# Kernel optimization log

Measured on AMD Instinct MI355X. Metric: run time of the kernel, lower is better.

Reference implementation:

```python
import jax, jax.numpy as jnp
import numpy as np

EPS_R2 = 1e-12
EPS_POS = 1e-08
EPS_SUM = 1e-12


def _gaussian_psf(k, sigma):
    ax = np.arange(-k // 2 + 1.0, k // 2 + 1.0)
    xx, yy = np.meshgrid(ax, ax)
    g = np.exp(-(xx ** 2 + yy ** 2) / (2.0 * sigma ** 2))
    g = g / g.sum()
    return jnp.asarray(g.astype(np.float32))[None, None]  # (1,1,k,k)


def setup_inputs() -> dict:
    key = jax.random.key(0)
    k1, k2, k3 = jax.random.split(key, 3)
    B, C, H, W = 16, 1, 1024, 1024
    src = jax.random.normal(k1, (B, C, H, W), dtype=jnp.float32)
    raw_psf = _gaussian_psf(21, 3.0) + 0.001 * jax.random.normal(k2, (1, 1, 21, 21), dtype=jnp.float32)
    sub = 0.1 * jax.random.normal(k3, (2,), dtype=jnp.float32)
    return {
        "src": src,
        "raw_psf": raw_psf,
        "x0": jnp.float32(0.0),
        "y0": jnp.float32(0.0),
        "raw_b": jnp.float32(0.08),
        "raw_rc": jnp.float32(0.01),
        "raw_subpix": sub,
    }


def _bilinear_sample(src, gx, gy):
    # src: (B,C,H,W); gx, gy: (B,Hg,Wg) normalized coords in [-1,1],
    # align_corners=True, zeros padding (matches F.grid_sample).
    B, C, H, W = src.shape
    ix = (gx + 1.0) * 0.5 * (W - 1)
    iy = (gy + 1.0) * 0.5 * (H - 1)
    ix0 = jnp.floor(ix)
    iy0 = jnp.floor(iy)
    wx1 = ix - ix0
    wy1 = iy - iy0
    ix0i = ix0.astype(jnp.int32)
    iy0i = iy0.astype(jnp.int32)
    ix1i = ix0i + 1
    iy1i = iy0i + 1
    bidx = jnp.arange(B)[:, None, None]

    def corner(yi, xi, w):
        valid = (yi >= 0) & (yi < H) & (xi >= 0) & (xi < W)
        yc = jnp.clip(yi, 0, H - 1)
        xc = jnp.clip(xi, 0, W - 1)
        v = src[bidx, :, yc, xc]  # (B,Hg,Wg,C)
        return v * (w * valid)[..., None]

    out = (corner(iy0i, ix0i, (1.0 - wy1) * (1.0 - wx1))
           + corner(iy0i, ix1i, (1.0 - wy1) * wx1)
           + corner(iy1i, ix0i, wy1 * (1.0 - wx1))
           + corner(iy1i, ix1i, wy1 * wx1))
    return jnp.transpose(out, (0, 3, 1, 2))  # (B,C,Hg,Wg)


def reference(src, raw_psf, x0, y0, raw_b, raw_rc, raw_subpix):
    B, C, H, W = src.shape
    k = raw_psf.shape[-1]
    b = jax.nn.softplus(raw_b) + EPS_POS
    rc = jax.nn.softplus(raw_rc) + EPS_POS
    sub = 0.25 * jnp.tanh(raw_subpix)

    xs = jnp.linspace(-1.0, 1.0, W)
    ys = jnp.linspace(-1.0, 1.0, H)
    # torch.meshgrid(ys, xs, indexing='xy') semantics: shape (W, H),
    # yv[i,j] = ys[j], xv[i,j] = xs[i] (note: transposed vs usual HxW).
    yv, xv = jnp.meshgrid(ys, xs, indexing='xy')

    dx = xv - x0
    dy = yv - y0
    denom = jnp.sqrt(dx * dx + dy * dy + EPS_R2 + rc * rc)
    ax = b * dx / denom
    ay = b * dy / denom

    gx = jnp.broadcast_to(xv - ax + sub[0], (B, W, H))
    gy = jnp.broadcast_to(yv - ay + sub[1], (B, W, H))

    y_warp = _bilinear_sample(src, gx, gy)  # (B,C,W,H)

    psf = jnp.maximum(raw_psf, 0.0)
    psf = psf / jnp.maximum(psf.sum(axis=(2, 3), keepdims=True), EPS_SUM)
    pad = k // 2
    y_conv = jax.lax.conv_general_dilated(
        y_warp, psf, window_strides=(1, 1),
        padding=((pad, pad), (pad, pad)),
        dimension_numbers=("NCHW", "OIHW", "NCHW"))
    return y_conv
```

## Files before the change

### kernel.cpp

```cpp
#include <hip/hip_runtime.h>
#include <math.h>

#define WW 1024
#define HH 1024
#define TI 64
#define TJ 128
#define HALO_J 148
#define VALID_I 84
#define FILL_I 96
#define PITCH_T 104
#define AOFF 448
#define AOFF2 21952
#define YOFF 43520
#define NEED_WS (174080u + 33554432u)

typedef short short8 __attribute__((ext_vector_type(8)));
typedef float float16 __attribute__((ext_vector_type(16)));

__device__ __forceinline__ unsigned short f2bf(float f) {
    union { float f; unsigned int u; } c; c.f = f;
    unsigned int u = c.u;
    return (unsigned short)((u + 0x7FFFu + ((u >> 16) & 1u)) >> 16);
}

__device__ __forceinline__ float warp_sample(const float* __restrict__ sb, int I, int J,
                                             float bpar, float rc2, float sub0, float sub1,
                                             float x0, float y0) {
    const float SSTEP = 2.0f / 1023.0f;
    float yv = fmaf((float)J, SSTEP, -1.0f);
    float xv = fmaf((float)I, SSTEP, -1.0f);
    float dx = xv - x0;
    float dy = yv - y0;
    float s = bpar * __builtin_amdgcn_rsqf(dx * dx + dy * dy + rc2);
    float gx = xv - dx * s + sub0;
    float gy = yv - dy * s + sub1;
    float ix = (gx + 1.0f) * (0.5f * 1023.0f);
    float iy = (gy + 1.0f) * (0.5f * 1023.0f);
    float fx = floorf(ix), fy = floorf(iy);
    float wx1 = ix - fx, wy1 = iy - fy;
    float wx0 = 1.f - wx1, wy0 = 1.f - wy1;
    int xi0 = (int)fx, yi0 = (int)fy;
    int xi1 = xi0 + 1, yi1 = yi0 + 1;
    int xc0 = min(max(xi0, 0), WW - 1);
    int xc1 = min(max(xi1, 0), WW - 1);
    int yc0 = min(max(yi0, 0), HH - 1);
    int yc1 = min(max(yi1, 0), HH - 1);
    bool vx0 = (unsigned)xi0 < WW, vx1 = (unsigned)xi1 < WW;
    bool vy0 = (unsigned)yi0 < HH, vy1 = (unsigned)yi1 < HH;
    float w00 = (vx0 && vy0) ? wy0 * wx0 : 0.f;
    float w01 = (vx1 && vy0) ? wy0 * wx1 : 0.f;
    float w10 = (vx0 && vy1) ? wy1 * wx0 : 0.f;
    float w11 = (vx1 && vy1) ? wy1 * wx1 : 0.f;
    float v00 = sb[yc0 * WW + xc0];
    float v01 = sb[yc0 * WW + xc1];
    float v10 = sb[yc1 * WW + xc0];
    float v11 = sb[yc1 * WW + xc1];
    return v00 * w00 + v01 * w01 + v10 * w10 + v11 * w11;
}

__global__ void prep_kernel(const float* __restrict__ raw_psf,
                            const float* __restrict__ x0p, const float* __restrict__ y0p,
                            const float* __restrict__ raw_b, const float* __restrict__ raw_rc,
                            const float* __restrict__ raw_sub,
                            float* __restrict__ ws) {
    __shared__ float red[512];
    __shared__ float psn[441];
    int t = threadIdx.x;
    float v = 0.f;
    if (t < 441) v = fmaxf(raw_psf[t], 0.f);
    red[t] = v;
    __syncthreads();
    for (int s = 256; s > 0; s >>= 1) {
        if (t < s) red[t] += red[t + s];
        __syncthreads();
    }
    float sum = fmaxf(red[0], 1e-12f);
    if (t < 441) { float pn = v / sum; ws[t] = pn; psn[t] = pn; }
    if (t == 0) {
        float b  = log1pf(expf(raw_b[0]))  + 1e-8f;
        float rc = log1pf(expf(raw_rc[0])) + 1e-8f;
        ws[441] = b;
        ws[442] = 1e-12f + rc * rc;
        ws[443] = 0.25f * tanhf(raw_sub[0]);
        ws[444] = 0.25f * tanhf(raw_sub[1]);
        ws[445] = x0p[0];
        ws[446] = y0p[0];
    }
    __syncthreads();

    short* A  = (short*)(ws + AOFF);
    short* A2 = (short*)(ws + AOFF2);
    for (int g = t; g < 21 * 256; g += 512) {
        int vv = g >> 8;
        int r  = g & 255;
        int d  = r >> 6;
        int l  = r & 63;
        int m  = l & 31;
        int k0 = (l >> 5) << 3;
        short8 o8, o8b;
#pragma unroll
        for (int q = 0; q < 8; ++q) {
            int u = 16 * d + k0 + q - m;
            unsigned short pv = 0, pv2 = 0;
            if ((unsigned)u <= 20u) pv = f2bf(psn[u * 21 + vv]);
            int u2 = u - 6;
            if ((unsigned)u2 <= 20u) pv2 = f2bf(psn[u2 * 21 + vv]);
            o8[q]  = (short)pv;
            o8b[q] = (short)pv2;
        }
        *(short8*)&A[(size_t)g * 8]  = o8;
        *(short8*)&A2[(size_t)g * 8] = o8b;
    }
}

__global__ __launch_bounds__(256, 4) void warp_kernel(
        const float* __restrict__ src, const float* __restrict__ pp,
        unsigned short* __restrict__ yw) {
    const float bpar = pp[441], rc2 = pp[442];
    const float sub0 = pp[443], sub1 = pp[444];
    const float x0 = pp[445], y0 = pp[446];
    const float SSTEP = 2.0f / 1023.0f;

    const int tid = threadIdx.x;
    const int nb  = blockIdx.x;
    const int b0  = nb >> 7;
    const int J0  = (nb & 127) << 3;
    const float* sb = src + ((size_t)b0 << 20);
    unsigned short* yb = yw + ((size_t)b0 << 20) + ((size_t)J0 << 10);

#pragma unroll 1
    for (int jr = 0; jr < 8; ++jr) {
        int J = J0 + jr;
        float yv = fmaf((float)J, SSTEP, -1.0f);
        float dy = yv - y0;
        float dyt = fmaf(dy, dy, rc2);
        unsigned short* yrow = yb + (jr << 10);

        float ixa[4], iya[4];
        bool bad = false;
#pragma unroll
        for (int q = 0; q < 4; ++q) {
            int I = (q << 8) + tid;
            float xv = fmaf((float)I, SSTEP, -1.0f);
            float dx = xv - x0;
            float s  = bpar * __builtin_amdgcn_rsqf(fmaf(dx, dx, dyt));
            float gx = xv - dx * s + sub0;
            float gy = yv - dy * s + sub1;
            ixa[q] = (gx + 1.0f) * (0.5f * 1023.0f);
            iya[q] = (gy + 1.0f) * (0.5f * 1023.0f);
            bad |= !(ixa[q] >= 0.f && ixa[q] < 1023.f &&
                     iya[q] >= 0.f && iya[q] < 1023.f);
        }
        if (!__any(bad)) {
            float v00[4], v01[4], v10[4], v11[4], fxs[4], fys[4];
#pragma unroll
            for (int q = 0; q < 4; ++q) {
                float fx = floorf(ixa[q]), fy = floorf(iya[q]);
                fxs[q] = fx; fys[q] = fy;
                const float* p = sb + (((int)fy) << 10) + (int)fx;
                v00[q] = p[0];
                v01[q] = p[1];
                v10[q] = p[WW];
                v11[q] = p[WW + 1];
            }
#pragma unroll
            for (int q = 0; q < 4; ++q) {
                float wx1 = ixa[q] - fxs[q];
                float wy1 = iya[q] - fys[q];
                float wx0 = 1.f - wx1;
                float r0 = fmaf(wx1, v01[q], wx0 * v00[q]);
                float r1 = fmaf(wx1, v11[q], wx0 * v10[q]);
                float val = fmaf(wy1, r1, (1.f - wy1) * r0);
                yrow[(q << 8) + tid] = f2bf(val);
            }
        } else {
#pragma unroll
            for (int q = 0; q < 4; ++q) {
                int I = (q << 8) + tid;
                float val = warp_sample(sb, I, J, bpar, rc2, sub0, sub1, x0, y0);
                yrow[(q << 8) + tid] = f2bf(val);
            }
        }
    }
}

__global__ __launch_bounds__(256, 5) void conv_kernel(
        const unsigned short* __restrict__ yw, const float* __restrict__ pp,
        float* __restrict__ out) {
    __shared__ unsigned short ThT[HALO_J * PITCH_T];

    const int tid = threadIdx.x;
    const int j0 = blockIdx.x * TJ;
    const int i0 = blockIdx.y * TI;
    const int b0 = blockIdx.z;

    const int lane = tid & 63;
    const int wv = tid >> 6;
    const int nrow = lane & 31;
    const int khalf = lane >> 5;

    const short8* Ap = ((const short8*)(pp + AOFF2)) + lane;
    short8 AfA[4], AfB[4];
#pragma unroll
    for (int d = 0; d < 4; ++d) AfA[d] = Ap[d * 64];
#pragma unroll
    for (int d = 0; d < 4; ++d) AfB[d] = Ap[256 + d * 64];

    const unsigned short* wb = yw + ((size_t)b0 << 20);

    for (int p = tid; p < HALO_J * 12; p += 256) {
        int hc = (int)((unsigned)p / 12u);
        int c  = p - hc * 12;
        int J  = j0 - 10 + hc;
        int xs = i0 - 16 + c * 8;
        short8 d8 = {0, 0, 0, 0, 0, 0, 0, 0};
        if ((unsigned)J < HH && (unsigned)xs < WW)
            d8 = *(const short8*)&wb[J * WW + xs];
        *(short8*)&ThT[hc * PITCH_T + c * 8] = d8;
    }
    __syncthreads();

    float16 acc[2];
#pragma unroll
    for (int m = 0; m < 2; ++m)
#pragma unroll
        for (int q = 0; q < 16; ++q) acc[m][q] = 0.f;

    const unsigned short* bpbase = &ThT[(32 * wv + nrow) * PITCH_T + khalf * 8];

#pragma unroll 1
    for (int v = 0; v < 20; v += 2) {
        {
            short8 Cur[4];
#pragma unroll
            for (int d = 0; d < 4; ++d) Cur[d] = AfA[d];
            int vp = v + 2;
#pragma unroll
            for (int d = 0; d < 4; ++d) AfA[d] = Ap[vp * 256 + d * 64];

            const unsigned short* bp = bpbase + v * PITCH_T;
            short8 Bf[6];
#pragma unroll
            for (int c = 0; c < 6; ++c) Bf[c] = *(const short8*)&bp[16 * c];
#pragma unroll
            for (int mq = 0; mq < 2; ++mq)
#pragma unroll
                for (int d = 0; d < 4; ++d)
                    acc[mq] = __builtin_amdgcn_mfma_f32_32x32x16_bf16(
                        Cur[d], Bf[2 * mq + d], acc[mq], 0, 0, 0);
        }
        {
            short8 Cur[4];
#pragma unroll
            for (int d = 0; d < 4; ++d) Cur[d] = AfB[d];
            int vp = v + 3; vp = vp > 20 ? 20 : vp;
#pragma unroll
            for (int d = 0; d < 4; ++d) AfB[d] = Ap[vp * 256 + d * 64];

            const unsigned short* bp = bpbase + (v + 1) * PITCH_T;
            short8 Bf[6];
#pragma unroll
            for (int c = 0; c < 6; ++c) Bf[c] = *(const short8*)&bp[16 * c];
#pragma unroll
            for (int mq = 0; mq < 2; ++mq)
#pragma unroll
                for (int d = 0; d < 4; ++d)
                    acc[mq] = __builtin_amdgcn_mfma_f32_32x32x16_bf16(
                        Cur[d], Bf[2 * mq + d], acc[mq], 0, 0, 0);
        }
    }
    {
        const unsigned short* bp = bpbase + 20 * PITCH_T;
        short8 Bf[6];
#pragma unroll
        for (int c = 0; c < 6; ++c) Bf[c] = *(const short8*)&bp[16 * c];
#pragma unroll
        for (int mq = 0; mq < 2; ++mq)
#pragma unroll
            for (int d = 0; d < 4; ++d)
                acc[mq] = __builtin_amdgcn_mfma_f32_32x32x16_bf16(
                    AfA[d], Bf[2 * mq + d], acc[mq], 0, 0, 0);
    }

    float* ob = out + (size_t)b0 * (WW * (size_t)HH);
    const int gj = j0 + 32 * wv + nrow;
#pragma unroll
    for (int mq = 0; mq < 2; ++mq) {
#pragma unroll
        for (int reg = 0; reg < 16; ++reg) {
            int row = (reg & 3) + 8 * (reg >> 2) + 4 * khalf;
            int gi = i0 + 32 * mq + row;
            ob[(size_t)gi * HH + gj] = acc[mq][reg];
        }
    }
}

__global__ __launch_bounds__(256, 4) void fused_kernel(
        const float* __restrict__ src, const float* __restrict__ pp,
        float* __restrict__ out) {
    __shared__ unsigned short ThT[HALO_J * PITCH_T];

    const int tid = threadIdx.x;
    const int j0 = blockIdx.x * TJ;
    const int i0 = blockIdx.y * TI;
    const int b0 = blockIdx.z;

    const float bpar = pp[441], rc2 = pp[442];
    const float sub0 = pp[443], sub1 = pp[444];
    const float x0 = pp[445], y0 = pp[446];

    const float* sb = src + (size_t)b0 * (HH * (size_t)WW);

    const int NELEM = HALO_J * FILL_I;
#pragma unroll 1
    for (int base = 0; base < NELEM; base += 1024) {
        float vals[4];
        int offs[4];
#pragma unroll
        for (int e = 0; e < 4; ++e) {
            int n = base + (e << 8) + tid;
            float val = 0.f;
            int off = -1;
            if (n < NELEM) {
                int hc = (int)((unsigned)n / 96u);
                int hr = n - hc * 96;
                off = hc * PITCH_T + hr;
                int J = j0 - 10 + hc;
                int I = i0 - 10 + hr;
                if (hr < VALID_I && (unsigned)J < HH && (unsigned)I < WW)
                    val = warp_sample(sb, I, J, bpar, rc2, sub0, sub1, x0, y0);
            }
            vals[e] = val;
            offs[e] = off;
        }
#pragma unroll
        for (int e = 0; e < 4; ++e) {
            if (offs[e] >= 0) ThT[offs[e]] = f2bf(vals[e]);
        }
    }
    __syncthreads();

    const int lane = tid & 63;
    const int wv = tid >> 6;
    const int nrow = lane & 31;
    const int khalf = lane >> 5;

    float16 acc[2];
#pragma unroll
    for (int m = 0; m < 2; ++m)
#pragma unroll
        for (int q = 0; q < 16; ++q) acc[m][q] = 0.f;

    const short8* Aall = (const short8*)(pp + AOFF);

#pragma unroll 1
    for (int v = 0; v < 21; ++v) {
        short8 Af[4];
#pragma unroll
        for (int d = 0; d < 4; ++d)
            Af[d] = Aall[(v * 4 + d) * 64 + lane];

        const unsigned short* bp = &ThT[(32 * wv + nrow + v) * PITCH_T + khalf * 8];
        short8 Bf[6];
#pragma unroll
        for (int c = 0; c < 6; ++c)
            Bf[c] = *(const short8*)&bp[16 * c];

#pragma unroll
        for (int mq = 0; mq < 2; ++mq) {
#pragma unroll
            for (int d = 0; d < 4; ++d)
                acc[mq] = __builtin_amdgcn_mfma_f32_32x32x16_bf16(
                    Af[d], Bf[2 * mq + d], acc[mq], 0, 0, 0);
        }
    }

    float* ob = out + (size_t)b0 * (WW * (size_t)HH);
    const int gj = j0 + 32 * wv + nrow;
#pragma unroll
    for (int mq = 0; mq < 2; ++mq) {
#pragma unroll
        for (int reg = 0; reg < 16; ++reg) {
            int row = (reg & 3) + 8 * (reg >> 2) + 4 * khalf;
            int gi = i0 + 32 * mq + row;
            ob[(size_t)gi * HH + gj] = acc[mq][reg];
        }
    }
}

extern "C" void kernel_launch(void* const* d_in, const int* in_sizes, int n_in,
                              void* d_out, int out_size, void* d_ws, size_t ws_size,
                              hipStream_t stream) {
    const float* src     = (const float*)d_in[0];
    const float* raw_psf = (const float*)d_in[1];
    const float* x0      = (const float*)d_in[2];
    const float* y0      = (const float*)d_in[3];
    const float* raw_b   = (const float*)d_in[4];
    const float* raw_rc  = (const float*)d_in[5];
    const float* raw_sub = (const float*)d_in[6];
    float* ws = (float*)d_ws;

    prep_kernel<<<1, 512, 0, stream>>>(raw_psf, x0, y0, raw_b, raw_rc, raw_sub, ws);

    dim3 grid(HH / TJ, WW / TI, 16);
    if (ws_size >= (size_t)NEED_WS) {
        unsigned short* yw = (unsigned short*)(ws + YOFF);
        warp_kernel<<<2048, 256, 0, stream>>>(src, ws, yw);
        conv_kernel<<<grid, 256, 0, stream>>>(yw, ws, (float*)d_out);
    } else {
        fused_kernel<<<grid, 256, 0, stream>>>(src, ws, (float*)d_out);
    }
}
```

Baseline: 191.0 us.

## Batch two rows per warp iteration and software-pipeline LDS loads in conv

The warp kernel now handles two output rows per iteration, issuing eight gather groups at once with a scheduling barrier so more global loads are in flight before the interpolation math. The conv kernel double-buffers its B fragments read from shared memory, loading the next row's fragments and A weights while the current MFMAs run, so LDS latency is hidden behind matrix work. Conv launch bounds drop from 5 to 4 waves per SIMD to leave room for the extra live registers. This raises register pressure and may reduce occupancy in both kernels.

```diff
diff --git a/kernel.cpp b/kernel.cpp
--- a/kernel.cpp
+++ b/kernel.cpp
@@ -129,62 +129,72 @@
     unsigned short* yb = yw + ((size_t)b0 << 20) + ((size_t)J0 << 10);
 
 #pragma unroll 1
-    for (int jr = 0; jr < 8; ++jr) {
-        int J = J0 + jr;
-        float yv = fmaf((float)J, SSTEP, -1.0f);
-        float dy = yv - y0;
-        float dyt = fmaf(dy, dy, rc2);
-        unsigned short* yrow = yb + (jr << 10);
-
-        float ixa[4], iya[4];
+    for (int jp = 0; jp < 4; ++jp) {
+        const int Jr = J0 + 2 * jp;
+        float yv0 = fmaf((float)Jr, SSTEP, -1.0f);
+        float yv1 = fmaf((float)(Jr + 1), SSTEP, -1.0f);
+        float dy0 = yv0 - y0, dy1 = yv1 - y0;
+        float dyt0 = fmaf(dy0, dy0, rc2), dyt1 = fmaf(dy1, dy1, rc2);
+        unsigned short* yrow0 = yb + ((2 * jp) << 10);
+        unsigned short* yrow1 = yrow0 + 1024;
+
+        float ixa[8], iya[8];
         bool bad = false;
 #pragma unroll
-        for (int q = 0; q < 4; ++q) {
+        for (int e = 0; e < 8; ++e) {
+            int r = e >> 2, q = e & 3;
             int I = (q << 8) + tid;
+            float yv  = r ? yv1 : yv0;
+            float dy  = r ? dy1 : dy0;
+            float dyt = r ? dyt1 : dyt0;
             float xv = fmaf((float)I, SSTEP, -1.0f);
             float dx = xv - x0;
             float s  = bpar * __builtin_amdgcn_rsqf(fmaf(dx, dx, dyt));
             float gx = xv - dx * s + sub0;
             float gy = yv - dy * s + sub1;
-            ixa[q] = (gx + 1.0f) * (0.5f * 1023.0f);
-            iya[q] = (gy + 1.0f) * (0.5f * 1023.0f);
-            bad |= !(ixa[q] >= 0.f && ixa[q] < 1023.f &&
-                     iya[q] >= 0.f && iya[q] < 1023.f);
+            ixa[e] = (gx + 1.0f) * (0.5f * 1023.0f);
+            iya[e] = (gy + 1.0f) * (0.5f * 1023.0f);
+            bad |= !(ixa[e] >= 0.f && ixa[e] < 1023.f &&
+                     iya[e] >= 0.f && iya[e] < 1023.f);
         }
         if (!__any(bad)) {
-            float v00[4], v01[4], v10[4], v11[4], fxs[4], fys[4];
-#pragma unroll
-            for (int q = 0; q < 4; ++q) {
-                float fx = floorf(ixa[q]), fy = floorf(iya[q]);
-                fxs[q] = fx; fys[q] = fy;
+            float v00[8], v01[8], v10[8], v11[8], fxs[8], fys[8];
+#pragma unroll
+            for (int e = 0; e < 8; ++e) {
+                float fx = floorf(ixa[e]), fy = floorf(iya[e]);
+                fxs[e] = fx; fys[e] = fy;
                 const float* p = sb + (((int)fy) << 10) + (int)fx;
-                v00[q] = p[0];
-                v01[q] = p[1];
-                v10[q] = p[WW];
-                v11[q] = p[WW + 1];
+                v00[e] = p[0];
+                v01[e] = p[1];
+                v10[e] = p[WW];
+                v11[e] = p[WW + 1];
             }
-#pragma unroll
-            for (int q = 0; q < 4; ++q) {
-                float wx1 = ixa[q] - fxs[q];
-                float wy1 = iya[q] - fys[q];
+            __builtin_amdgcn_sched_barrier(0);
+#pragma unroll
+            for (int e = 0; e < 8; ++e) {
+                float wx1 = ixa[e] - fxs[e];
+                float wy1 = iya[e] - fys[e];
                 float wx0 = 1.f - wx1;
-                float r0 = fmaf(wx1, v01[q], wx0 * v00[q]);
-                float r1 = fmaf(wx1, v11[q], wx0 * v10[q]);
+                float r0 = fmaf(wx1, v01[e], wx0 * v00[e]);
+                float r1 = fmaf(wx1, v11[e], wx0 * v10[e]);
                 float val = fmaf(wy1, r1, (1.f - wy1) * r0);
-                yrow[(q << 8) + tid] = f2bf(val);
+                unsigned short* yr = (e >> 2) ? yrow1 : yrow0;
+                yr[((e & 3) << 8) + tid] = f2bf(val);
             }
         } else {
 #pragma unroll
-            for (int q = 0; q < 4; ++q) {
-                int I = (q << 8) + tid;
+            for (int e = 0; e < 8; ++e) {
+                int I = ((e & 3) << 8) + tid;
+                int J = Jr + (e >> 2);
                 float val = warp_sample(sb, I, J, bpar, rc2, sub0, sub1, x0, y0);
-                yrow[(q << 8) + tid] = f2bf(val);
+                unsigned short* yr = (e >> 2) ? yrow1 : yrow0;
+                yr[((e & 3) << 8) + tid] = f2bf(val);
             }
         }
     }
 }
 
-__global__ __launch_bounds__(256, 5) void conv_kernel(
+__global__ __launch_bounds__(256, 4) void conv_kernel(
         const unsigned short* __restrict__ yw, const float* __restrict__ pp,
         float* __restrict__ out) {
     __shared__ unsigned short ThT[HALO_J * PITCH_T];
@@ -228,59 +238,61 @@
 
     const unsigned short* bpbase = &ThT[(32 * wv + nrow) * PITCH_T + khalf * 8];
 
+    short8 BfA[6], BfB[6];
+#pragma unroll
+    for (int c = 0; c < 6; ++c) BfA[c] = *(const short8*)&bpbase[16 * c];
+#pragma unroll
+    for (int c = 0; c < 6; ++c) BfB[c] = *(const short8*)&bpbase[PITCH_T + 16 * c];
+
 #pragma unroll 1
-    for (int v = 0; v < 20; v += 2) {
-        {
-            short8 Cur[4];
-#pragma unroll
-            for (int d = 0; d < 4; ++d) Cur[d] = AfA[d];
-            int vp = v + 2;
-#pragma unroll
-            for (int d = 0; d < 4; ++d) AfA[d] = Ap[vp * 256 + d * 64];
-
-            const unsigned short* bp = bpbase + v * PITCH_T;
-            short8 Bf[6];
-#pragma unroll
-            for (int c = 0; c < 6; ++c) Bf[c] = *(const short8*)&bp[16 * c];
-#pragma unroll
-            for (int mq = 0; mq < 2; ++mq)
-#pragma unroll
-                for (int d = 0; d < 4; ++d)
-                    acc[mq] = __builtin_amdgcn_mfma_f32_32x32x16_bf16(
-                        Cur[d], Bf[2 * mq + d], acc[mq], 0, 0, 0);
-        }
-        {
-            short8 Cur[4];
-#pragma unroll
-            for (int d = 0; d < 4; ++d) Cur[d] = AfB[d];
-            int vp = v + 3; vp = vp > 20 ? 20 : vp;
-#pragma unroll
-            for (int d = 0; d < 4; ++d) AfB[d] = Ap[vp * 256 + d * 64];
-
-            const unsigned short* bp = bpbase + (v + 1) * PITCH_T;
-            short8 Bf[6];
-#pragma unroll
-            for (int c = 0; c < 6; ++c) Bf[c] = *(const short8*)&bp[16 * c];
-#pragma unroll
-            for (int mq = 0; mq < 2; ++mq)
-#pragma unroll
-                for (int d = 0; d < 4; ++d)
-                    acc[mq] = __builtin_amdgcn_mfma_f32_32x32x16_bf16(
-                        Cur[d], Bf[2 * mq + d], acc[mq], 0, 0, 0);
-        }
-    }
-    {
-        const unsigned short* bp = bpbase + 20 * PITCH_T;
-        short8 Bf[6];
-#pragma unroll
-        for (int c = 0; c < 6; ++c) Bf[c] = *(const short8*)&bp[16 * c];
+    for (int v = 0; v < 18; v += 2) {
 #pragma unroll
         for (int mq = 0; mq < 2; ++mq)
 #pragma unroll
             for (int d = 0; d < 4; ++d)
                 acc[mq] = __builtin_amdgcn_mfma_f32_32x32x16_bf16(
-                    AfA[d], Bf[2 * mq + d], acc[mq], 0, 0, 0);
-    }
+                    AfA[d], BfA[2 * mq + d], acc[mq], 0, 0, 0);
+#pragma unroll
+        for (int c = 0; c < 6; ++c)
+            BfA[c] = *(const short8*)&bpbase[(v + 2) * PITCH_T + 16 * c];
+#pragma unroll
+        for (int d = 0; d < 4; ++d) AfA[d] = Ap[(v + 2) * 256 + d * 64];
+
+#pragma unroll
+        for (int mq = 0; mq < 2; ++mq)
+#pragma unroll
+            for (int d = 0; d < 4; ++d)
+                acc[mq] = __builtin_amdgcn_mfma_f32_32x32x16_bf16(
+                    AfB[d], BfB[2 * mq + d], acc[mq], 0, 0, 0);
+#pragma unroll
+        for (int c = 0; c < 6; ++c)
+            BfB[c] = *(const short8*)&bpbase[(v + 3) * PITCH_T + 16 * c];
+#pragma unroll
+        for (int d = 0; d < 4; ++d) AfB[d] = Ap[(v + 3) * 256 + d * 64];
+    }
+#pragma unroll
+    for (int mq = 0; mq < 2; ++mq)
+#pragma unroll
+        for (int d = 0; d < 4; ++d)
+            acc[mq] = __builtin_amdgcn_mfma_f32_32x32x16_bf16(
+                AfA[d], BfA[2 * mq + d], acc[mq], 0, 0, 0);
+#pragma unroll
+    for (int c = 0; c < 6; ++c)
+        BfA[c] = *(const short8*)&bpbase[20 * PITCH_T + 16 * c];
+#pragma unroll
+    for (int d = 0; d < 4; ++d) AfA[d] = Ap[20 * 256 + d * 64];
+#pragma unroll
+    for (int mq = 0; mq < 2; ++mq)
+#pragma unroll
+        for (int d = 0; d < 4; ++d)
+            acc[mq] = __builtin_amdgcn_mfma_f32_32x32x16_bf16(
+                AfB[d], BfB[2 * mq + d], acc[mq], 0, 0, 0);
+#pragma unroll
+    for (int mq = 0; mq < 2; ++mq)
+#pragma unroll
+        for (int d = 0; d < 4; ++d)
+            acc[mq] = __builtin_amdgcn_mfma_f32_32x32x16_bf16(
+                AfA[d], BfA[2 * mq + d], acc[mq], 0, 0, 0);
 
     float* ob = out + (size_t)b0 * (WW * (size_t)HH);
     const int gj = j0 + 32 * wv + nrow;
```

Result: no change. 194.1 us (+1.6%).
